# Kernel tuning notes

Measured on AMD Instinct MI355X. Metric: run time of the kernel, lower is better.

Reference implementation:

```python
import jax, jax.numpy as jnp
import numpy as np

B, S, D, H = 4, 2048, 1024, 16
DK = D // H


def setup_inputs() -> dict:
    key = jax.random.key(0)
    ks = jax.random.split(key, 10)
    s = 0.02  # keep linear outputs well-scaled
    causal = jnp.triu(jnp.ones((S, S), dtype=bool), k=1)  # True = masked
    return {
        "Q": jax.random.normal(ks[0], (B, S, D), dtype=jnp.float32),
        "K_V": jax.random.normal(ks[1], (B, S, D), dtype=jnp.float32),
        "mask": jnp.broadcast_to(causal, (B, S, S)),
        "Wq": jax.random.normal(ks[2], (D, D), dtype=jnp.float32) * s,
        "bq": jnp.zeros((D,), dtype=jnp.float32),
        "Wk": jax.random.normal(ks[3], (D, D), dtype=jnp.float32) * s,
        "bk": jnp.zeros((D,), dtype=jnp.float32),
        "Wv": jax.random.normal(ks[4], (D, D), dtype=jnp.float32) * s,
        "bv": jnp.zeros((D,), dtype=jnp.float32),
        "Wo": jax.random.normal(ks[5], (D, D), dtype=jnp.float32) * s,
        "bo": jnp.zeros((D,), dtype=jnp.float32),
    }


def reference(Q, K_V, mask, Wq, bq, Wk, bk, Wv, bv, Wo, bo):
    # Linear projections
    q = Q @ Wq + bq          # [B, Sq, D]
    k = K_V @ Wk + bk        # [B, Sk, D]
    v = K_V @ Wv + bv        # [B, Sk, D]
    Sq, Sk = q.shape[1], k.shape[1]
    # chunk(dim=2)+cat(dim=0) == split into H heads of size DK
    q = q.reshape(B, Sq, H, DK)
    k = k.reshape(B, Sk, H, DK)
    v = v.reshape(B, Sk, H, DK)
    scale = 1.0 / jnp.sqrt(jnp.float32(DK))
    scores = jnp.einsum("bqhd,bkhd->bhqk", q, k) * scale  # [B,H,Sq,Sk]
    # mask.repeat(head_num,1,1) == broadcast mask over heads
    scores = jnp.where(mask[:, None, :, :], -jnp.inf, scores)
    attn = jax.nn.softmax(scores, axis=-1)
    # dropout is identity in eval mode
    out = jnp.einsum("bhqk,bkhd->bqhd", attn, v).reshape(B, Sq, D)
    return out @ Wo + bo
```

## Files before the change

kernel.cpp:

```cpp
#include <hip/hip_runtime.h>

typedef unsigned short u16;
typedef __attribute__((ext_vector_type(8))) __bf16 bf16x8;
typedef __attribute__((ext_vector_type(4))) float f32x4;

#define B_  4
#define S_  2048
#define D_  1024
#define H_  16
#define DK_ 64

__device__ __forceinline__ u16 f2bf(float f) {
  unsigned u = __float_as_uint(f);
  u += 0x7fffu + ((u >> 16) & 1u);
  return (u16)(u >> 16);
}
__device__ __forceinline__ float hexp2(float f) {
  return __builtin_amdgcn_exp2f(f);
}
__device__ __forceinline__ unsigned pack_bf2(float f0, float f1) {
  return __builtin_amdgcn_perm(__float_as_uint(f1), __float_as_uint(f0), 0x07060302u);
}

__device__ __forceinline__ void load_lds16(const u16* g, u16* l) {
  __builtin_amdgcn_global_load_lds((const __attribute__((address_space(1))) void*)g,
                                   (__attribute__((address_space(3))) void*)l,
                                   16, 0, 0);
}

__global__ void cvt_bf16_2(const float* __restrict__ x0, u16* __restrict__ y0,
                           const float* __restrict__ x1, u16* __restrict__ y1, int n4) {
  int i = blockIdx.x * blockDim.x + threadIdx.x;
  const float* x = x0; u16* y = y0;
  int j = i;
  if (i >= n4) { x = x1; y = y1; j = i - n4; }
  float4 v = ((const float4*)x)[j];
  ushort4 o;
  o.x = f2bf(v.x); o.y = f2bf(v.y); o.z = f2bf(v.z); o.w = f2bf(v.w);
  ((ushort4*)y)[j] = o;
}

__global__ void transpose_cvt4(const float* __restrict__ W0, const float* __restrict__ W1,
                               const float* __restrict__ W2, const float* __restrict__ W3,
                               u16* __restrict__ T0, u16* __restrict__ T1,
                               u16* __restrict__ T2, u16* __restrict__ T3) {
  __shared__ float tile[32][33];
  const float* W = (blockIdx.z == 0) ? W0 : (blockIdx.z == 1) ? W1 : (blockIdx.z == 2) ? W2 : W3;
  u16*         T = (blockIdx.z == 0) ? T0 : (blockIdx.z == 1) ? T1 : (blockIdx.z == 2) ? T2 : T3;
  int bx = blockIdx.x * 32, by = blockIdx.y * 32;
  int tx = threadIdx.x, ty = threadIdx.y;
  #pragma unroll
  for (int i = 0; i < 32; i += 8)
    tile[ty + i][tx] = W[(size_t)(by + ty + i) * D_ + bx + tx];
  __syncthreads();
  #pragma unroll
  for (int i = 0; i < 32; i += 8)
    T[(size_t)(bx + ty + i) * D_ + by + tx] = f2bf(tile[tx][ty + i]);
}

#define GBM 128
#define GBN 256
#define GNT 16

template<int MODE>
__global__ __launch_bounds__(512, 2)
void gemm8p(const u16* __restrict__ Aq, const u16* __restrict__ Ak,
            const u16* __restrict__ Bt,
            const float* __restrict__ bq, const float* __restrict__ bk,
            const float* __restrict__ bv,
            u16* __restrict__ qp, u16* __restrict__ kp, u16* __restrict__ vpT,
            float* __restrict__ Cf, float qscale) {
  __shared__ __align__(16) u16 sm[2 * 24576];
  const int tid  = threadIdx.x;
  const int lane = tid & 63, wave = tid >> 6;
  const int bm = blockIdx.x * GBM;
  const int bn = blockIdx.y * GBN;
  const int wm = (wave >> 2) * 64, wn = (wave & 3) * 64;
  const int fm = lane & 15, fk4 = lane >> 4;
  const int K = D_;

  int path = 0;
  const u16* A = Aq;
  if constexpr (MODE == 0) { path = bn >> 10; if (path != 0) A = Ak; }

  const int sr  = tid >> 2;
  const int sl  = tid & 3;
  const int kof = sl * 8;
  const u16* gA  = A  + (size_t)(bm + sr) * K + kof;
  const u16* gB0 = Bt + (size_t)(bn + sr) * K + kof;
  const u16* gB1 = Bt + (size_t)(bn + 128 + sr) * K + kof;

#define GR(t, ks) do { \
    u16* lr_ = &sm[((t) & 1) * 24576 + (ks) * 12288]; \
    const int ko_ = (t) * 64 + (ks) * 32; \
    load_lds16(gA  + ko_, lr_ + tid * 8); \
    load_lds16(gB0 + ko_, lr_ + 4096 + tid * 8); \
    load_lds16(gB1 + ko_, lr_ + 8192 + tid * 8); \
  } while (0)

  f32x4 acc[4][4] = {};

  GR(0, 0);
  asm volatile("" ::: "memory");
  GR(0, 1);
  asm volatile("" ::: "memory");
  GR(1, 0);

  #pragma unroll
  for (int t = 0; t < GNT; ++t) {
    #pragma unroll
    for (int ks = 0; ks < 2; ++ks) {
      if (t < GNT - 1)  asm volatile("s_waitcnt vmcnt(6)" ::: "memory");
      else if (ks == 0) asm volatile("s_waitcnt vmcnt(3)" ::: "memory");
      else              asm volatile("s_waitcnt vmcnt(0)" ::: "memory");
      __builtin_amdgcn_s_barrier();
      if (ks == 0) { if (t + 1 < GNT) GR(t + 1, 1); }
      else         { if (t + 2 < GNT) GR(t + 2, 0); }
      asm volatile("" ::: "memory");

      const u16* rb = &sm[(t & 1) * 24576 + ks * 12288];
      bf16x8 af[4], bfr[4];
      #pragma unroll
      for (int m = 0; m < 4; ++m)
        af[m] = *(const bf16x8*)&rb[(wm + m * 16 + fm) * 32 + fk4 * 8];
      #pragma unroll
      for (int j = 0; j < 4; ++j)
        bfr[j] = *(const bf16x8*)&rb[(128 + wn + j * 16 + fm) * 32 + fk4 * 8];
      __builtin_amdgcn_s_setprio(1);
      #pragma unroll
      for (int m = 0; m < 4; ++m)
        #pragma unroll
        for (int j = 0; j < 4; ++j)
          acc[m][j] = __builtin_amdgcn_mfma_f32_16x16x32_bf16(af[m], bfr[j], acc[m][j], 0, 0, 0);
      __builtin_amdgcn_s_setprio(0);
    }
  }
#undef GR

  if constexpr (MODE == 0) {
    #pragma unroll
    for (int i = 0; i < 4; ++i) {
      #pragma unroll
      for (int j = 0; j < 4; ++j) {
        int colg = bn + wn + j * 16 + fm;
        int rowg0 = bm + wm + i * 16 + fk4 * 4;
        if (path == 0) {
          float bb = bq[colg];
          #pragma unroll
          for (int rg = 0; rg < 4; ++rg)
            qp[(size_t)(rowg0 + rg) * D_ + colg] = f2bf((acc[i][j][rg] + bb) * qscale);
        } else if (path == 1) {
          int ck = colg - 1024;
          float bb = bk[ck];
          #pragma unroll
          for (int rg = 0; rg < 4; ++rg)
            kp[(size_t)(rowg0 + rg) * D_ + ck] = f2bf(acc[i][j][rg] + bb);
        } else {
          int cv = colg - 2048;
          float bb = bv[cv];
          int hh = cv >> 6, dk = cv & 63;
          int bbt = rowg0 >> 11, s = rowg0 & (S_ - 1);
          ushort4 pk4;
          pk4.x = f2bf(acc[i][j][0] + bb);
          pk4.y = f2bf(acc[i][j][1] + bb);
          pk4.z = f2bf(acc[i][j][2] + bb);
          pk4.w = f2bf(acc[i][j][3] + bb);
          *(ushort4*)&vpT[(((size_t)bbt * H_ + hh) * DK_ + dk) * S_ + s] = pk4;
        }
      }
    }
  } else {
    #pragma unroll
    for (int i = 0; i < 4; ++i)
      #pragma unroll
      for (int j = 0; j < 4; ++j) {
        int colg = bn + wn + j * 16 + fm;
        float bb = bq[colg];
        #pragma unroll
        for (int rg = 0; rg < 4; ++rg) {
          int rowg = bm + wm + i * 16 + fk4 * 4 + rg;
          Cf[(size_t)rowg * D_ + colg] = acc[i][j][rg] + bb;
        }
      }
  }
}

__global__ __launch_bounds__(256, 4)
void attn_kernel(const u16* __restrict__ qp, const u16* __restrict__ kp,
                 const u16* __restrict__ vpT, u16* __restrict__ ao) {
  __shared__ u16 Ks[2][8 * 512];
  __shared__ u16 Vs[2][8 * 512];
  __shared__ u16 Ps[4][512];

  const int tid  = threadIdx.x;
  const int lane = tid & 63;
  const int w    = tid >> 6;
  const int fm   = lane & 15;
  const int fk4  = lane >> 4;
  const int csl  = (lane ^ ((lane >> 3) & 7)) * 8;

  const int i = blockIdx.x;
  const int p = i >> 6;
  const int bh = i & 63;
  const int b  = bh >> 4;
  const int h  = bh & 15;

  const u16* kb = kp  + (size_t)(b * S_) * D_ + h * DK_;
  const u16* vb = vpT + (size_t)((b * H_ + h) * DK_) * S_;

  bf16x8 vones;
  #pragma unroll
  for (int e = 0; e < 8; ++e) vones[e] = (__bf16)1.0f;

#define STAGEKV(bf, jj) do { \
    const int kv0_ = (jj) * 64; \
    _Pragma("unroll") \
    for (int c = 0; c < 2; ++c) { \
      int idx = 2 * w + c;                    \
      load_lds16(kb + (size_t)(kv0_ + (idx >> 1) * 16 + fm) * D_ + (idx & 1) * 32 + fk4 * 8, \
                 &Ks[bf][idx * 512 + lane * 8]); \
    } \
    _Pragma("unroll") \
    for (int c = 0; c < 2; ++c) { \
      int idx = 2 * w + c;                    \
      load_lds16(vb + (size_t)((idx & 3) * 16 + fm) * S_ + kv0_ + (idx >> 2) * 32 + fk4 * 8, \
                 &Vs[bf][idx * 512 + lane * 8]); \
    } } while (0)

  #pragma unroll 1
  for (int sidx = 0; sidx < 2; ++sidx) {
    const int qt = (sidx == 0) ? p : 31 - p;
    const int q0 = qt * 64 + w * 16;
    const int nj = qt + 1;

    bf16x8 aq[2];
    #pragma unroll
    for (int kh = 0; kh < 2; ++kh)
      aq[kh] = *(const bf16x8*)(qp + (size_t)(b * S_ + q0 + fm) * D_
                                   + h * DK_ + kh * 32 + fk4 * 8);

    f32x4 oacc[4] = {};
    f32x4 lacc = {0.f, 0.f, 0.f, 0.f};

    __builtin_amdgcn_s_barrier();
    STAGEKV(0, 0);

    #pragma unroll 1
    for (int j = 0; j < nj; ++j) {
      const int kv0 = j * 64;
      const bool lastt = (j == nj - 1);

      __builtin_amdgcn_s_barrier();
      if (j + 1 < nj) {
        STAGEKV((j + 1) & 1, j + 1);
        asm volatile("s_waitcnt vmcnt(4)" ::: "memory");
      } else {
        asm volatile("s_waitcnt vmcnt(0)" ::: "memory");
      }
      __builtin_amdgcn_s_barrier();

      const u16* Kb_ = &Ks[j & 1][0];
      const u16* Vb_ = &Vs[j & 1][0];

      #pragma unroll
      for (int kth = 0; kth < 2; ++kth) {
        #pragma unroll
        for (int mtl = 0; mtl < 2; ++mtl) {
          const int mt = kth * 2 + mtl;
          bf16x8 kf0 = *(const bf16x8*)&Kb_[(mt * 2 + 0) * 512 + lane * 8];
          bf16x8 kf1 = *(const bf16x8*)&Kb_[(mt * 2 + 1) * 512 + lane * 8];
          f32x4 z = {0.f, 0.f, 0.f, 0.f};
          __builtin_amdgcn_s_setprio(1);
          z = __builtin_amdgcn_mfma_f32_16x16x32_bf16(kf0, aq[0], z, 0, 0, 0);
          z = __builtin_amdgcn_mfma_f32_16x16x32_bf16(kf1, aq[1], z, 0, 0, 0);
          __builtin_amdgcn_s_setprio(0);

          const int kvr = kv0 + mt * 16 + fk4 * 4;
          float e[4];
          #pragma unroll
          for (int rg = 0; rg < 4; ++rg) {
            float zz = z[rg];
            if (lastt && (kvr + rg > q0 + fm)) zz = -1e30f;
            e[rg] = hexp2(zz);
          }
          const int fk4c = (mt & 1) * 2 + (fk4 >> 1);
          const int c    = fk4c * 16 + fm;
          const int woff = (c ^ ((c >> 3) & 7)) * 8 + (fk4 & 1) * 4;
          uint2 wv;
          wv.x = pack_bf2(e[0], e[1]); wv.y = pack_bf2(e[2], e[3]);
          *(uint2*)&Ps[w][woff] = wv;
        }

        bf16x8 ap = *(const bf16x8*)&Ps[w][csl];
        __builtin_amdgcn_s_setprio(1);
        #pragma unroll
        for (int nt = 0; nt < 4; ++nt) {
          bf16x8 bv = *(const bf16x8*)&Vb_[(kth * 4 + nt) * 512 + lane * 8];
          oacc[nt] = __builtin_amdgcn_mfma_f32_16x16x32_bf16(ap, bv, oacc[nt], 0, 0, 0);
        }
        lacc = __builtin_amdgcn_mfma_f32_16x16x32_bf16(ap, vones, lacc, 0, 0, 0);
        __builtin_amdgcn_s_setprio(0);
      }
    }

    #pragma unroll
    for (int rg = 0; rg < 4; ++rg) {
      float inv = 1.0f / lacc[rg];
      int q = q0 + fk4 * 4 + rg;
      #pragma unroll
      for (int nt = 0; nt < 4; ++nt) {
        float o = oacc[nt][rg] * inv;
        ao[(size_t)(b * S_ + q) * D_ + h * DK_ + nt * 16 + fm] = f2bf(o);
      }
    }
  }
#undef STAGEKV
}

extern "C" void kernel_launch(void* const* d_in, const int* in_sizes, int n_in,
                              void* d_out, int out_size, void* d_ws, size_t ws_size,
                              hipStream_t stream) {
  const float* Q  = (const float*)d_in[0];
  const float* KV = (const float*)d_in[1];
  const float* Wq = (const float*)d_in[3];
  const float* bq = (const float*)d_in[4];
  const float* Wk = (const float*)d_in[5];
  const float* bk = (const float*)d_in[6];
  const float* Wv = (const float*)d_in[7];
  const float* bv = (const float*)d_in[8];
  const float* Wo = (const float*)d_in[9];
  const float* bo = (const float*)d_in[10];
  float* out = (float*)d_out;

  char* ws = (char*)d_ws;
  u16* Qb  = (u16*)(ws);
  u16* Kb  = (u16*)(ws + (16ull << 20));
  u16* Wqt = (u16*)(ws + (32ull << 20));
  u16* Wkt = (u16*)(ws + (34ull << 20));
  u16* Wvt = (u16*)(ws + (36ull << 20));
  u16* Wot = (u16*)(ws + (38ull << 20));
  u16* qp  = (u16*)(ws + (40ull << 20));
  u16* kp  = (u16*)(ws + (56ull << 20));
  u16* vpT = (u16*)(ws + (72ull << 20));
  u16* ao  = Qb;

  const int n4 = (B_ * S_ * D_) / 4;
  cvt_bf16_2<<<2 * n4 / 256, 256, 0, stream>>>(Q, Qb, KV, Kb, n4);

  transpose_cvt4<<<dim3(32, 32, 4), dim3(32, 8), 0, stream>>>(Wq, Wk, Wv, Wo,
                                                              Wqt, Wkt, Wvt, Wot);

  const float qscale = 0.125f * 1.44269504f;
  gemm8p<0><<<dim3(8192 / GBM, 3072 / GBN), 512, 0, stream>>>(
      Qb, Kb, Wqt, bq, bk, bv, qp, kp, vpT, nullptr, qscale);

  attn_kernel<<<1024, 256, 0, stream>>>(qp, kp, vpT, ao);

  gemm8p<1><<<dim3(8192 / GBM, 1024 / GBN), 512, 0, stream>>>(
      ao, nullptr, Wot, bo, nullptr, nullptr, nullptr, nullptr, nullptr, out, 1.0f);
}
```

Baseline: 336.2 us.

## Enlarge attention query tile to 256 rows with four query fragments per wave

Restructures the attention kernel so each block handles a 256-row query tile (64 rows per wave, as four 16-row fragments) instead of two 64-row tiles paired for causal balance. Each K/V tile staged in LDS is now reused across four query fragments, which cuts global K/V traffic and the number of barriers per unit of work. Waves whose diagonal has already passed skip compute but still join the staging barriers. The cost is more registers (launch bounds lowered to 3), fewer blocks (512), and some idle waves in causal tiles, which reduces occupancy and can unbalance load.

```diff
diff --git a/kernel.cpp b/kernel.cpp
--- a/kernel.cpp
+++ b/kernel.cpp
@@ -185,12 +185,12 @@
   }
 }
 
-__global__ __launch_bounds__(256, 4)
+__global__ __launch_bounds__(256, 3)
 void attn_kernel(const u16* __restrict__ qp, const u16* __restrict__ kp,
                  const u16* __restrict__ vpT, u16* __restrict__ ao) {
   __shared__ u16 Ks[2][8 * 512];
   __shared__ u16 Vs[2][8 * 512];
-  __shared__ u16 Ps[4][512];
+  __shared__ u16 Ps[4][4 * 512];
 
   const int tid  = threadIdx.x;
   const int lane = tid & 63;
@@ -199,11 +199,16 @@
   const int fk4  = lane >> 4;
   const int csl  = (lane ^ ((lane >> 3) & 7)) * 8;
 
-  const int i = blockIdx.x;
-  const int p = i >> 6;
-  const int bh = i & 63;
+  const int x  = blockIdx.x;
+  const int dh = x & 255;
+  const int bh = dh >> 2;
   const int b  = bh >> 4;
   const int h  = bh & 15;
+  const int qt = (x < 256) ? 7 - (dh & 3) : (dh & 3);
+
+  const int q0 = qt * 256 + w * 64;
+  const int nj = (qt + 1) * 4;
+  const int jd = qt * 4 + w;
 
   const u16* kb = kp  + (size_t)(b * S_) * D_ + h * DK_;
   const u16* vb = vpT + (size_t)((b * H_ + h) * DK_) * S_;
@@ -227,94 +232,104 @@
                  &Vs[bf][idx * 512 + lane * 8]); \
     } } while (0)
 
+  bf16x8 aq[4][2];
+  #pragma unroll
+  for (int qf = 0; qf < 4; ++qf)
+    #pragma unroll
+    for (int kh = 0; kh < 2; ++kh)
+      aq[qf][kh] = *(const bf16x8*)(qp + (size_t)(b * S_ + q0 + qf * 16 + fm) * D_
+                                       + h * DK_ + kh * 32 + fk4 * 8);
+
+  f32x4 oacc[4][4] = {};
+  f32x4 lacc[4] = {};
+
+  STAGEKV(0, 0);
+
   #pragma unroll 1
-  for (int sidx = 0; sidx < 2; ++sidx) {
-    const int qt = (sidx == 0) ? p : 31 - p;
-    const int q0 = qt * 64 + w * 16;
-    const int nj = qt + 1;
-
-    bf16x8 aq[2];
-    #pragma unroll
-    for (int kh = 0; kh < 2; ++kh)
-      aq[kh] = *(const bf16x8*)(qp + (size_t)(b * S_ + q0 + fm) * D_
-                                   + h * DK_ + kh * 32 + fk4 * 8);
-
-    f32x4 oacc[4] = {};
-    f32x4 lacc = {0.f, 0.f, 0.f, 0.f};
-
+  for (int j = 0; j < nj; ++j) {
     __builtin_amdgcn_s_barrier();
-    STAGEKV(0, 0);
-
-    #pragma unroll 1
-    for (int j = 0; j < nj; ++j) {
-      const int kv0 = j * 64;
-      const bool lastt = (j == nj - 1);
-
-      __builtin_amdgcn_s_barrier();
-      if (j + 1 < nj) {
-        STAGEKV((j + 1) & 1, j + 1);
-        asm volatile("s_waitcnt vmcnt(4)" ::: "memory");
-      } else {
-        asm volatile("s_waitcnt vmcnt(0)" ::: "memory");
-      }
-      __builtin_amdgcn_s_barrier();
-
-      const u16* Kb_ = &Ks[j & 1][0];
-      const u16* Vb_ = &Vs[j & 1][0];
-
-      #pragma unroll
-      for (int kth = 0; kth < 2; ++kth) {
-        #pragma unroll
-        for (int mtl = 0; mtl < 2; ++mtl) {
-          const int mt = kth * 2 + mtl;
-          bf16x8 kf0 = *(const bf16x8*)&Kb_[(mt * 2 + 0) * 512 + lane * 8];
-          bf16x8 kf1 = *(const bf16x8*)&Kb_[(mt * 2 + 1) * 512 + lane * 8];
-          f32x4 z = {0.f, 0.f, 0.f, 0.f};
-          __builtin_amdgcn_s_setprio(1);
-          z = __builtin_amdgcn_mfma_f32_16x16x32_bf16(kf0, aq[0], z, 0, 0, 0);
-          z = __builtin_amdgcn_mfma_f32_16x16x32_bf16(kf1, aq[1], z, 0, 0, 0);
-          __builtin_amdgcn_s_setprio(0);
-
-          const int kvr = kv0 + mt * 16 + fk4 * 4;
+    if (j + 1 < nj) {
+      STAGEKV((j + 1) & 1, j + 1);
+      asm volatile("s_waitcnt vmcnt(4)" ::: "memory");
+    } else {
+      asm volatile("s_waitcnt vmcnt(0)" ::: "memory");
+    }
+    __builtin_amdgcn_s_barrier();
+
+    if (j > jd) continue;
+    const bool lastt = (j == jd);
+    const int kv0 = j * 64;
+    const u16* Kb_ = &Ks[j & 1][0];
+    const u16* Vb_ = &Vs[j & 1][0];
+
+    #pragma unroll
+    for (int kth = 0; kth < 2; ++kth) {
+      #pragma unroll
+      for (int mtl = 0; mtl < 2; ++mtl) {
+        const int mt = kth * 2 + mtl;
+        bf16x8 kf0 = *(const bf16x8*)&Kb_[(mt * 2 + 0) * 512 + lane * 8];
+        bf16x8 kf1 = *(const bf16x8*)&Kb_[(mt * 2 + 1) * 512 + lane * 8];
+        f32x4 z[4] = {};
+        __builtin_amdgcn_s_setprio(1);
+        #pragma unroll
+        for (int qf = 0; qf < 4; ++qf) {
+          z[qf] = __builtin_amdgcn_mfma_f32_16x16x32_bf16(kf0, aq[qf][0], z[qf], 0, 0, 0);
+          z[qf] = __builtin_amdgcn_mfma_f32_16x16x32_bf16(kf1, aq[qf][1], z[qf], 0, 0, 0);
+        }
+        __builtin_amdgcn_s_setprio(0);
+
+        const int kvr = kv0 + mt * 16 + fk4 * 4;
+        const int fk4c = mtl * 2 + (fk4 >> 1);
+        const int c    = fk4c * 16 + fm;
+        const int woff = (c ^ ((c >> 3) & 7)) * 8 + (fk4 & 1) * 4;
+        #pragma unroll
+        for (int qf = 0; qf < 4; ++qf) {
           float e[4];
           #pragma unroll
           for (int rg = 0; rg < 4; ++rg) {
-            float zz = z[rg];
-            if (lastt && (kvr + rg > q0 + fm)) zz = -1e30f;
+            float zz = z[qf][rg];
+            if (lastt && (kvr + rg > q0 + qf * 16 + fm)) zz = -1e30f;
             e[rg] = hexp2(zz);
           }
-          const int fk4c = (mt & 1) * 2 + (fk4 >> 1);
-          const int c    = fk4c * 16 + fm;
-          const int woff = (c ^ ((c >> 3) & 7)) * 8 + (fk4 & 1) * 4;
           uint2 wv;
           wv.x = pack_bf2(e[0], e[1]); wv.y = pack_bf2(e[2], e[3]);
-          *(uint2*)&Ps[w][woff] = wv;
+          *(uint2*)&Ps[w][qf * 512 + woff] = wv;
         }
-
-        bf16x8 ap = *(const bf16x8*)&Ps[w][csl];
-        __builtin_amdgcn_s_setprio(1);
-        #pragma unroll
-        for (int nt = 0; nt < 4; ++nt) {
-          bf16x8 bv = *(const bf16x8*)&Vb_[(kth * 4 + nt) * 512 + lane * 8];
-          oacc[nt] = __builtin_amdgcn_mfma_f32_16x16x32_bf16(ap, bv, oacc[nt], 0, 0, 0);
-        }
-        lacc = __builtin_amdgcn_mfma_f32_16x16x32_bf16(ap, vones, lacc, 0, 0, 0);
-        __builtin_amdgcn_s_setprio(0);
-      }
-    }
-
-    #pragma unroll
-    for (int rg = 0; rg < 4; ++rg) {
-      float inv = 1.0f / lacc[rg];
-      int q = q0 + fk4 * 4 + rg;
+      }
+
+      bf16x8 ap[4];
+      #pragma unroll
+      for (int qf = 0; qf < 4; ++qf)
+        ap[qf] = *(const bf16x8*)&Ps[w][qf * 512 + csl];
+      __builtin_amdgcn_s_setprio(1);
       #pragma unroll
       for (int nt = 0; nt < 4; ++nt) {
-        float o = oacc[nt][rg] * inv;
-        ao[(size_t)(b * S_ + q) * D_ + h * DK_ + nt * 16 + fm] = f2bf(o);
-      }
+        bf16x8 bv = *(const bf16x8*)&Vb_[(kth * 4 + nt) * 512 + lane * 8];
+        #pragma unroll
+        for (int qf = 0; qf < 4; ++qf)
+          oacc[qf][nt] = __builtin_amdgcn_mfma_f32_16x16x32_bf16(ap[qf], bv, oacc[qf][nt], 0, 0, 0);
+      }
+      #pragma unroll
+      for (int qf = 0; qf < 4; ++qf)
+        lacc[qf] = __builtin_amdgcn_mfma_f32_16x16x32_bf16(ap[qf], vones, lacc[qf], 0, 0, 0);
+      __builtin_amdgcn_s_setprio(0);
     }
   }
 #undef STAGEKV
+
+  #pragma unroll
+  for (int qf = 0; qf < 4; ++qf) {
+    #pragma unroll
+    for (int rg = 0; rg < 4; ++rg) {
+      float inv = 1.0f / lacc[qf][rg];
+      int q = q0 + qf * 16 + fk4 * 4 + rg;
+      #pragma unroll
+      for (int nt = 0; nt < 4; ++nt) {
+        float o = oacc[qf][nt][rg] * inv;
+        ao[(size_t)(b * S_ + q) * D_ + h * DK_ + nt * 16 + fm] = f2bf(o);
+      }
+    }
+  }
 }
 
 extern "C" void kernel_launch(void* const* d_in, const int* in_sizes, int n_in,
@@ -354,7 +369,7 @@
   gemm8p<0><<<dim3(8192 / GBM, 3072 / GBN), 512, 0, stream>>>(
       Qb, Kb, Wqt, bq, bk, bv, qp, kp, vpT, nullptr, qscale);
 
-  attn_kernel<<<1024, 256, 0, stream>>>(qp, kp, vpT, ao);
+  attn_kernel<<<512, 256, 0, stream>>>(qp, kp, vpT, ao);
 
   gemm8p<1><<<dim3(8192 / GBM, 1024 / GBN), 512, 0, stream>>>(
       ao, nullptr, Wot, bo, nullptr, nullptr, nullptr, nullptr, nullptr, out, 1.0f);
```

After: 351.7 us. 1.05x slower.
